# Kernel optimization log

Hardware: AMD Instinct MI355X
Metric: run time of the kernel (lower is better)

The kernel has to match this reference:

```python
import jax, jax.numpy as jnp
import numpy as np

VOCAB = 32000
ROUTE_BIAS = 10.0  # weight on the deterministic one-hot route vs mu logits


def setup_inputs() -> dict:
    key = jax.random.key(0)
    k1, k2, k3, k4, k5, k6 = jax.random.split(key, 6)
    B, S, H = 2, 4096, 1024
    E, Ie = 8, 512  # intermediate_size=4096 -> expert_intermediate=512, fused dim=2*Ie=1024
    return {
        "hidden_states": jax.random.normal(k1, (B, S, H), dtype=jnp.float32),
        "token_ids": jax.random.randint(k2, (B, S), 0, VOCAB),
        "mu": jax.random.normal(k3, (B, S, H), dtype=jnp.float32),
        "gate_up_proj": jax.random.normal(k4, (E, H, 2 * Ie), dtype=jnp.float32) * 0.02,
        "down_proj": jax.random.normal(k5, (E, Ie, H), dtype=jnp.float32) * 0.02,
        "mu_router_w": jax.random.normal(k6, (E, H), dtype=jnp.float32) * 0.02,
    }


def reference(hidden_states, token_ids, mu, gate_up_proj, down_proj, mu_router_w):
    B, S, H = hidden_states.shape
    E, _, F2 = gate_up_proj.shape
    Ie = F2 // 2
    N = B * S

    # deterministic token->expert routing, optionally perturbed by mu logits
    token_to_expert = jnp.arange(VOCAB, dtype=jnp.int32) % E
    base_expert = token_to_expert[jnp.clip(token_ids, 0, VOCAB - 1)]      # [B,S]
    mu_logits = jnp.einsum('bsh,eh->bse', mu, mu_router_w)                 # [B,S,E]
    combined = jax.nn.one_hot(base_expert, E, dtype=mu_logits.dtype) * ROUTE_BIAS + mu_logits
    expert_ids = jnp.argmax(combined, axis=-1).reshape(N)                  # [N]

    x = hidden_states.reshape(N, H)
    tok = jnp.arange(N)

    # compute per-expert GEMM then select per-token expert output
    # (same math as gathering the full weight slab per token, without the
    #  N*H*2Ie gathered-weight blowup of the original torch code)
    gu_all = jnp.einsum('nh,ehf->enf', x, gate_up_proj)                    # [E,N,2Ie]
    gu = gu_all[expert_ids, tok]                                           # [N,2Ie]
    gate, up = gu[:, :Ie], gu[:, Ie:]
    inter = jax.nn.silu(gate) * up                                         # [N,Ie]

    z_all = jnp.einsum('ni,eih->enh', inter, down_proj)                    # [E,N,H]
    out = z_all[expert_ids, tok].reshape(B, S, H)
    return out
```

## Files before the change

kernel.cpp:

```cpp
#include <hip/hip_runtime.h>
#include <hip/hip_bf16.h>
#include <stdint.h>

typedef __bf16 bf16x8 __attribute__((ext_vector_type(8)));
typedef float f32x4 __attribute__((ext_vector_type(4)));

#define ROUTE_BIAS_F 10.0f
#define VOCAB_SZ 32000

__device__ __forceinline__ unsigned short f2bf(float f) {
    union { float f; unsigned u; } v; v.f = f;
    unsigned u = v.u;
    unsigned r = u + 0x7FFFu + ((u >> 16) & 1u);
    return (unsigned short)(r >> 16);
}
__device__ __forceinline__ float bf2f(unsigned short s) {
    union { unsigned u; float f; } v; v.u = ((unsigned)s) << 16;
    return v.f;
}
__device__ __forceinline__ void ld16(const unsigned short* g, unsigned short* l) {
    __builtin_amdgcn_global_load_lds(
        (const __attribute__((address_space(1))) void*)g,
        (__attribute__((address_space(3))) void*)l, 16, 0, 0);
}

__global__ void k_prep(const float* __restrict__ hidden, const float* __restrict__ mu,
                       const int* __restrict__ tok_ids, const float* __restrict__ rw,
                       unsigned short* __restrict__ xb, int* __restrict__ eids,
                       int H, int N) {
    int lane = threadIdx.x & 63;
    int wv   = threadIdx.x >> 6;
    int tok  = blockIdx.x * 4 + wv;
    if (tok >= N) return;
    const float4* hp = (const float4*)(hidden + (size_t)tok * H);
    const float4* mp = (const float4*)(mu + (size_t)tok * H);
    const float4* rp = (const float4*)rw;
    ushort4* xp = (ushort4*)(xb + (size_t)tok * H);
    int H4 = H >> 2;
    float acc[8];
#pragma unroll
    for (int e = 0; e < 8; ++e) acc[e] = 0.f;
#pragma unroll
    for (int j = 0; j < 4; ++j) {
        int idx = lane + 64 * j;
        float4 h4 = hp[idx];
        ushort4 o;
        o.x = f2bf(h4.x); o.y = f2bf(h4.y); o.z = f2bf(h4.z); o.w = f2bf(h4.w);
        xp[idx] = o;
        float4 m4 = mp[idx];
#pragma unroll
        for (int e = 0; e < 8; ++e) {
            float4 w4 = rp[e * H4 + idx];
            acc[e] += m4.x * w4.x + m4.y * w4.y + m4.z * w4.z + m4.w * w4.w;
        }
    }
#pragma unroll
    for (int e = 0; e < 8; ++e) {
        float v = acc[e];
#pragma unroll
        for (int off = 32; off > 0; off >>= 1) v += __shfl_xor(v, off);
        acc[e] = v;
    }
    if (lane == 0) {
        int t = tok_ids[tok];
        if (t < 0) t = 0;
        if (t > VOCAB_SZ - 1) t = VOCAB_SZ - 1;
        int be = t % 8;
        float best = -1e30f; int bi = 0;
#pragma unroll
        for (int e = 0; e < 8; ++e) {
            float v = acc[e] + (e == be ? ROUTE_BIAS_F : 0.f);
            if (v > best) { best = v; bi = e; }
        }
        eids[tok] = bi;
    }
}

__global__ __launch_bounds__(256) void k_transpose_all(
        const float* __restrict__ gup, const float* __restrict__ dnp,
        unsigned short* __restrict__ wgut, unsigned short* __restrict__ wdnt,
        int H, int F2, int Ie) {
    __shared__ float tile[64][65];
    int z = blockIdx.z;
    const float* inp; unsigned short* outp; int R, C;
    if (z < 8) { R = H; C = F2; inp = gup + (size_t)z * R * C;       outp = wgut + (size_t)z * R * C; }
    else       { R = Ie; C = H; inp = dnp + (size_t)(z - 8) * R * C; outp = wdnt + (size_t)(z - 8) * R * C; }
    int c0 = blockIdx.x * 64, r0 = blockIdx.y * 64;
    if (r0 >= R) return;
    int tid = threadIdx.x;
    int tr = tid >> 4;
    int tc = (tid & 15) * 4;
#pragma unroll
    for (int p = 0; p < 4; ++p) {
        float4 v = *(const float4*)&inp[(size_t)(r0 + tr + 16 * p) * C + c0 + tc];
        tile[tr + 16 * p][tc + 0] = v.x;
        tile[tr + 16 * p][tc + 1] = v.y;
        tile[tr + 16 * p][tc + 2] = v.z;
        tile[tr + 16 * p][tc + 3] = v.w;
    }
    __syncthreads();
#pragma unroll
    for (int p = 0; p < 4; ++p) {
        int c = tr + 16 * p;
        ushort4 o;
        o.x = f2bf(tile[tc + 0][c]);
        o.y = f2bf(tile[tc + 1][c]);
        o.z = f2bf(tile[tc + 2][c]);
        o.w = f2bf(tile[tc + 3][c]);
        *(ushort4*)&outp[(size_t)(c0 + c) * R + r0 + tc] = o;
    }
}

__global__ void k_count(const int* __restrict__ eids,
                        int* __restrict__ blockcnt, int N) {
    __shared__ int cnt[8];
    int tid = threadIdx.x;
    if (tid < 8) cnt[tid] = 0;
    __syncthreads();
    int tok = blockIdx.x * 256 + tid;
    int lane = tid & 63;
    int eid = (tok < N) ? eids[tok] : -1;
#pragma unroll
    for (int e = 0; e < 8; ++e) {
        unsigned long long m = __ballot(eid == e);
        if (lane == 0 && m) atomicAdd(&cnt[e], __popcll(m));
    }
    __syncthreads();
    if (tid < 8) blockcnt[blockIdx.x * 8 + tid] = cnt[tid];
}

__global__ void k_scan(const int* __restrict__ blockcnt,
                       int* __restrict__ counts, int* __restrict__ base_,
                       int* __restrict__ offs, int NB) {
    __shared__ int tot[8];
    int lane = threadIdx.x;
    int e = lane >> 3, g = lane & 7;
    int v[4];
    int s = 0;
#pragma unroll
    for (int i = 0; i < 4; ++i) { v[i] = s; s += blockcnt[(g * 4 + i) * 8 + e]; }
    int inc = s;
#pragma unroll
    for (int d = 1; d < 8; d <<= 1) {
        int t = __shfl_up(inc, d);
        if (g >= d) inc += t;
    }
    int excl = inc - s;
#pragma unroll
    for (int i = 0; i < 4; ++i) offs[(g * 4 + i) * 8 + e] = excl + v[i];
    if (g == 7) { counts[e] = inc; tot[e] = inc; }
    __syncthreads();
    if (lane == 0) {
        int s2 = 0;
#pragma unroll
        for (int i = 0; i < 8; ++i) { base_[i] = s2; s2 += tot[i]; }
    }
}

__global__ void k_scatter(const int* __restrict__ eids,
                          const int* __restrict__ offs,
                          int* __restrict__ list, int N) {
    __shared__ int wavecnt[4][8];
    int tid = threadIdx.x;
    int lane = tid & 63, wv = tid >> 6;
    int tok = blockIdx.x * 256 + tid;
    int eid = (tok < N) ? eids[tok] : -1;
    unsigned long long below = (1ull << lane) - 1ull;
    int myrank = 0;
#pragma unroll
    for (int e = 0; e < 8; ++e) {
        unsigned long long m = __ballot(eid == e);
        if (lane == 0) wavecnt[wv][e] = __popcll(m);
        if (eid == e) myrank = __popcll(m & below);
    }
    __syncthreads();
    if (eid >= 0) {
        int pre = 0;
        for (int w = 0; w < wv; ++w) pre += wavecnt[w][eid];
        int pos = offs[blockIdx.x * 8 + eid] + pre + myrank;
        list[eid * N + pos] = tok;
    }
}

#define TM 128
#define TN 128
#define TK 64

__global__ __launch_bounds__(256, 2) void k_gemm_gateup(
    const unsigned short* __restrict__ X,
    const unsigned short* __restrict__ Wt,
    unsigned short* __restrict__ IT,
    const int* __restrict__ counts, const int* __restrict__ base_,
    const int* __restrict__ list, int N, int H, int Ie) {
    int bid = blockIdx.x;
    int e = bid & 7;
    int t = bid >> 3;
    int nt = t & 7;
    int slot = t >> 3;
    int cnt = counts[e];
    int F2 = 2 * Ie;
    int b = base_[e];
    int nt64 = nt * 64;

    __shared__ __align__(16) unsigned short As[2][TM * TK];
    __shared__ __align__(16) unsigned short Bs[2][TN * TK];

    int tid = threadIdx.x;
    int lane = tid & 63, wv = tid >> 6;
    int wr = (wv >> 1) * 64;
    int wc = (wv & 1) * 64;

    int rowg = lane >> 3;
    int sl   = (lane & 7) ^ rowg;

    const unsigned short* bg[4];
#pragma unroll
    for (int i = 0; i < 4; ++i) {
        int r = wv * 32 + i * 8 + rowg;
        int wrow = (r & 1) * Ie + nt64 + (r >> 1);
        bg[i] = Wt + ((size_t)e * F2 + wrow) * H + sl * 8;
    }

    int q = lane >> 4, m = lane & 15;
    int sw = m & 7;
    int nk = H / TK;

    for (int mt = slot; mt * TM < cnt; mt += 8) {
        int m0 = mt * TM;

        const unsigned short* ag[4];
#pragma unroll
        for (int i = 0; i < 4; ++i) {
            int r = wv * 32 + i * 8 + rowg;
            int gr = m0 + r;
            int tokrow = (gr < cnt) ? list[e * N + gr] : 0;
            ag[i] = X + (size_t)tokrow * H + sl * 8;
        }

        f32x4 acc[4][4];
#pragma unroll
        for (int i = 0; i < 4; ++i)
#pragma unroll
            for (int j = 0; j < 4; ++j) acc[i][j] = (f32x4)(0.f);

#pragma unroll
        for (int i = 0; i < 4; ++i) ld16(ag[i], &As[0][(wv * 32 + i * 8) * TK]);
#pragma unroll
        for (int i = 0; i < 4; ++i) ld16(bg[i], &Bs[0][(wv * 32 + i * 8) * TK]);
        __syncthreads();

        int cur = 0;
        for (int t_ = 0; t_ < nk; ++t_) {
            if (t_ + 1 < nk) {
                int k1 = (t_ + 1) * TK;
#pragma unroll
                for (int i = 0; i < 4; ++i) ld16(ag[i] + k1, &As[cur ^ 1][(wv * 32 + i * 8) * TK]);
#pragma unroll
                for (int i = 0; i < 4; ++i) ld16(bg[i] + k1, &Bs[cur ^ 1][(wv * 32 + i * 8) * TK]);
            }
            const unsigned short* Ac = As[cur];
            const unsigned short* Bc = Bs[cur];
            __builtin_amdgcn_s_setprio(1);
#pragma unroll
            for (int ks = 0; ks < TK; ks += 32) {
                int kc = ks >> 3;
                int ck = ((kc + q) ^ sw) << 3;
                bf16x8 af[4], bfr[4];
#pragma unroll
                for (int im = 0; im < 4; ++im)
                    af[im] = *(const bf16x8*)&Ac[(wr + m + im * 16) * TK + ck];
#pragma unroll
                for (int in_ = 0; in_ < 4; ++in_)
                    bfr[in_] = *(const bf16x8*)&Bc[(wc + m + in_ * 16) * TK + ck];
#pragma unroll
                for (int im = 0; im < 4; ++im)
#pragma unroll
                    for (int in_ = 0; in_ < 4; ++in_)
                        acc[im][in_] = __builtin_amdgcn_mfma_f32_16x16x32_bf16(
                            af[im], bfr[in_], acc[im][in_], 0, 0, 0);
            }
            __builtin_amdgcn_s_setprio(0);
            __syncthreads();
            cur ^= 1;
        }

#pragma unroll
        for (int im = 0; im < 4; ++im) {
#pragma unroll
            for (int j = 0; j < 4; ++j) {
                int row = wr + im * 16 + q * 4 + j;
                int gr = m0 + row;
#pragma unroll
                for (int in_ = 0; in_ < 4; ++in_) {
                    float v = acc[im][in_][j];
                    float u = __shfl_xor(v, 1);
                    float g = v;
                    float s = g / (1.f + __expf(-g));
                    float res = s * u;
                    if (!(lane & 1) && gr < cnt) {
                        int oc = nt64 + ((wc + in_ * 16 + m) >> 1);
                        IT[(size_t)(b + gr) * Ie + oc] = f2bf(res);
                    }
                }
            }
        }
    }
}

__global__ __launch_bounds__(256, 3) void k_gemm_down(
    const unsigned short* __restrict__ IT,
    const unsigned short* __restrict__ Wt,
    float* __restrict__ OUT,
    const int* __restrict__ counts, const int* __restrict__ base_,
    const int* __restrict__ list, int N, int Ie, int H) {
    int bid = blockIdx.x;
    int e = bid & 7;
    int t = bid >> 3;
    int nt = t & 7;
    int slot = t >> 3;
    int cnt = counts[e];
    int n0 = nt * TN;
    int b = base_[e];

    __shared__ __align__(16) unsigned short As[TM * TK];
    __shared__ __align__(16) unsigned short Bs[TN * TK];

    int tid = threadIdx.x;
    int lane = tid & 63, wv = tid >> 6;
    int wr = (wv >> 1) * 64;
    int wc = (wv & 1) * 64;

    int rowg = lane >> 3;
    int sl   = (lane & 7) ^ rowg;

    const unsigned short* We = Wt + ((size_t)e * H + n0) * Ie;
    const unsigned short* bg[4];
#pragma unroll
    for (int i = 0; i < 4; ++i) {
        int r = wv * 32 + i * 8 + rowg;
        bg[i] = We + (size_t)r * Ie + sl * 8;
    }

    int q = lane >> 4, m = lane & 15;
    int sw = m & 7;

    for (int mt = slot; mt * TM < cnt; mt += 8) {
        int m0 = mt * TM;

        const unsigned short* ag[4];
#pragma unroll
        for (int i = 0; i < 4; ++i) {
            int r = wv * 32 + i * 8 + rowg;
            int gr = m0 + r;
            int arow = (gr < cnt) ? (b + gr) : b;
            ag[i] = IT + (size_t)arow * Ie + sl * 8;
        }

        f32x4 acc[4][4];
#pragma unroll
        for (int i = 0; i < 4; ++i)
#pragma unroll
            for (int j = 0; j < 4; ++j) acc[i][j] = (f32x4)(0.f);

        for (int k0 = 0; k0 < Ie; k0 += TK) {
#pragma unroll
            for (int i = 0; i < 4; ++i)
                ld16(ag[i] + k0, &As[(wv * 32 + i * 8) * TK]);
#pragma unroll
            for (int i = 0; i < 4; ++i)
                ld16(bg[i] + k0, &Bs[(wv * 32 + i * 8) * TK]);
            __syncthreads();
#pragma unroll
            for (int ks = 0; ks < TK; ks += 32) {
                int kc = ks >> 3;
                int ck = ((kc + q) ^ sw) << 3;
                bf16x8 af[4], bfr[4];
#pragma unroll
                for (int im = 0; im < 4; ++im)
                    af[im] = *(const bf16x8*)&As[(wr + m + im * 16) * TK + ck];
#pragma unroll
                for (int in_ = 0; in_ < 4; ++in_)
                    bfr[in_] = *(const bf16x8*)&Bs[(wc + m + in_ * 16) * TK + ck];
#pragma unroll
                for (int im = 0; im < 4; ++im)
#pragma unroll
                    for (int in_ = 0; in_ < 4; ++in_)
                        acc[im][in_] = __builtin_amdgcn_mfma_f32_16x16x32_bf16(
                            af[im], bfr[in_], acc[im][in_], 0, 0, 0);
            }
            __syncthreads();
        }

#pragma unroll
        for (int im = 0; im < 4; ++im) {
#pragma unroll
            for (int j = 0; j < 4; ++j) {
                int row = wr + im * 16 + q * 4 + j;
                int gr = m0 + row;
                if (gr < cnt) {
                    int tok = list[e * N + gr];
                    float* orow = OUT + (size_t)tok * H + n0;
#pragma unroll
                    for (int in_ = 0; in_ < 4; ++in_) {
                        int col = wc + in_ * 16 + m;
                        orow[col] = acc[im][in_][j];
                    }
                }
            }
        }
    }
}

extern "C" void kernel_launch(void* const* d_in, const int* in_sizes, int n_in,
                              void* d_out, int out_size, void* d_ws, size_t ws_size,
                              hipStream_t stream) {
    const float* hidden   = (const float*)d_in[0];
    const int*   tok_ids  = (const int*)d_in[1];
    const float* mu       = (const float*)d_in[2];
    const float* gup      = (const float*)d_in[3];
    const float* dnp      = (const float*)d_in[4];
    const float* rw       = (const float*)d_in[5];
    float* out = (float*)d_out;

    int N  = in_sizes[1];
    int H  = in_sizes[0] / N;
    int E  = in_sizes[5] / H;
    int F2 = in_sizes[3] / (E * H);
    int Ie = F2 / 2;

    int NB = (N + 255) / 256;

    char* ws = (char*)d_ws;
    size_t o = 0;
    auto alloc = [&](size_t sz) {
        size_t r = o;
        o += (sz + 255) & ~(size_t)255;
        return r;
    };
    int* counts   = (int*)(ws + alloc((size_t)E * 4));
    int* base_    = (int*)(ws + alloc((size_t)E * 4));
    int* eids     = (int*)(ws + alloc((size_t)N * 4));
    int* blockcnt = (int*)(ws + alloc((size_t)NB * 8 * 4));
    int* offs     = (int*)(ws + alloc((size_t)NB * 8 * 4));
    int* list     = (int*)(ws + alloc((size_t)E * N * 4));
    unsigned short* xb   = (unsigned short*)(ws + alloc((size_t)N * H * 2));
    unsigned short* wgut = (unsigned short*)(ws + alloc((size_t)E * F2 * H * 2));
    unsigned short* wdnt = (unsigned short*)(ws + alloc((size_t)E * H * Ie * 2));
    unsigned short* it   = (unsigned short*)(ws + alloc((size_t)N * Ie * 2));

    k_prep<<<dim3((N + 3) / 4), dim3(256), 0, stream>>>(hidden, mu, tok_ids, rw, xb, eids, H, N);

    k_transpose_all<<<dim3(16, 16, 16), dim3(256), 0, stream>>>(gup, dnp, wgut, wdnt, H, F2, Ie);

    k_count<<<dim3(NB), dim3(256), 0, stream>>>(eids, blockcnt, N);
    k_scan<<<dim3(1), dim3(64), 0, stream>>>(blockcnt, counts, base_, offs, NB);
    k_scatter<<<dim3(NB), dim3(256), 0, stream>>>(eids, offs, list, N);

    k_gemm_gateup<<<dim3(E * (Ie / 64) * 8), dim3(256), 0, stream>>>(
        xb, wgut, it, counts, base_, list, N, H, Ie);

    k_gemm_down<<<dim3(E * (H / TN) * 8), dim3(256), 0, stream>>>(
        it, wdnt, out, counts, base_, list, N, Ie, H);
}
```

Before: 239.1 us.

## Prefetch two K-tiles ahead with register-staged fragments in both MoE GEMMs

Both GEMM kernels now issue global-to-LDS loads two tiles ahead. They wait with an explicit vmcnt count instead of a full syncthreads, load all fragments for the tile into registers, then refill the freed LDS buffer before running the MFMAs. The down-projection kernel gains double-buffered LDS and its occupancy hint drops from 3 to 2 blocks per CU. The aim is to hide global load latency behind MFMA work, at the cost of more registers and LDS per block.

```diff
diff --git a/kernel.cpp b/kernel.cpp
--- a/kernel.cpp
+++ b/kernel.cpp
@@ -13,10 +13,6 @@
     unsigned u = v.u;
     unsigned r = u + 0x7FFFu + ((u >> 16) & 1u);
     return (unsigned short)(r >> 16);
-}
-__device__ __forceinline__ float bf2f(unsigned short s) {
-    union { unsigned u; float f; } v; v.u = ((unsigned)s) << 16;
-    return v.f;
 }
 __device__ __forceinline__ void ld16(const unsigned short* g, unsigned short* l) {
     __builtin_amdgcn_global_load_lds(
@@ -244,45 +240,54 @@
             for (int j = 0; j < 4; ++j) acc[i][j] = (f32x4)(0.f);
 
 #pragma unroll
-        for (int i = 0; i < 4; ++i) ld16(ag[i], &As[0][(wv * 32 + i * 8) * TK]);
-#pragma unroll
-        for (int i = 0; i < 4; ++i) ld16(bg[i], &Bs[0][(wv * 32 + i * 8) * TK]);
-        __syncthreads();
-
-        int cur = 0;
+        for (int i = 0; i < 4; ++i) ld16(ag[i],      &As[0][(wv * 32 + i * 8) * TK]);
+#pragma unroll
+        for (int i = 0; i < 4; ++i) ld16(bg[i],      &Bs[0][(wv * 32 + i * 8) * TK]);
+#pragma unroll
+        for (int i = 0; i < 4; ++i) ld16(ag[i] + TK, &As[1][(wv * 32 + i * 8) * TK]);
+#pragma unroll
+        for (int i = 0; i < 4; ++i) ld16(bg[i] + TK, &Bs[1][(wv * 32 + i * 8) * TK]);
+
         for (int t_ = 0; t_ < nk; ++t_) {
-            if (t_ + 1 < nk) {
-                int k1 = (t_ + 1) * TK;
-#pragma unroll
-                for (int i = 0; i < 4; ++i) ld16(ag[i] + k1, &As[cur ^ 1][(wv * 32 + i * 8) * TK]);
-#pragma unroll
-                for (int i = 0; i < 4; ++i) ld16(bg[i] + k1, &Bs[cur ^ 1][(wv * 32 + i * 8) * TK]);
+            asm volatile("s_waitcnt vmcnt(8)" ::: "memory");
+            __builtin_amdgcn_s_barrier();
+
+            const unsigned short* Ac = As[t_ & 1];
+            const unsigned short* Bc = Bs[t_ & 1];
+            bf16x8 af[2][4], bfr[2][4];
+#pragma unroll
+            for (int s = 0; s < 2; ++s) {
+                int ck = (((s * 4) + q) ^ sw) << 3;
+#pragma unroll
+                for (int im = 0; im < 4; ++im)
+                    af[s][im] = *(const bf16x8*)&Ac[(wr + m + im * 16) * TK + ck];
+#pragma unroll
+                for (int in_ = 0; in_ < 4; ++in_)
+                    bfr[s][in_] = *(const bf16x8*)&Bc[(wc + m + in_ * 16) * TK + ck];
             }
-            const unsigned short* Ac = As[cur];
-            const unsigned short* Bc = Bs[cur];
+            asm volatile("s_waitcnt lgkmcnt(0)" ::: "memory");
+            __builtin_amdgcn_s_barrier();
+
+            int tn = t_ + 2; if (tn > nk - 1) tn = nk - 1;
+            int kk = tn * TK;
+#pragma unroll
+            for (int i = 0; i < 4; ++i) ld16(ag[i] + kk, &As[t_ & 1][(wv * 32 + i * 8) * TK]);
+#pragma unroll
+            for (int i = 0; i < 4; ++i) ld16(bg[i] + kk, &Bs[t_ & 1][(wv * 32 + i * 8) * TK]);
+
             __builtin_amdgcn_s_setprio(1);
 #pragma unroll
-            for (int ks = 0; ks < TK; ks += 32) {
-                int kc = ks >> 3;
-                int ck = ((kc + q) ^ sw) << 3;
-                bf16x8 af[4], bfr[4];
-#pragma unroll
-                for (int im = 0; im < 4; ++im)
-                    af[im] = *(const bf16x8*)&Ac[(wr + m + im * 16) * TK + ck];
-#pragma unroll
-                for (int in_ = 0; in_ < 4; ++in_)
-                    bfr[in_] = *(const bf16x8*)&Bc[(wc + m + in_ * 16) * TK + ck];
+            for (int s = 0; s < 2; ++s)
 #pragma unroll
                 for (int im = 0; im < 4; ++im)
 #pragma unroll
                     for (int in_ = 0; in_ < 4; ++in_)
                         acc[im][in_] = __builtin_amdgcn_mfma_f32_16x16x32_bf16(
-                            af[im], bfr[in_], acc[im][in_], 0, 0, 0);
-            }
+                            af[s][im], bfr[s][in_], acc[im][in_], 0, 0, 0);
             __builtin_amdgcn_s_setprio(0);
-            __syncthreads();
-            cur ^= 1;
-        }
+        }
+        asm volatile("s_waitcnt vmcnt(0)" ::: "memory");
+        __builtin_amdgcn_s_barrier();
 
 #pragma unroll
         for (int im = 0; im < 4; ++im) {
@@ -307,7 +312,7 @@
     }
 }
 
-__global__ __launch_bounds__(256, 3) void k_gemm_down(
+__global__ __launch_bounds__(256, 2) void k_gemm_down(
     const unsigned short* __restrict__ IT,
     const unsigned short* __restrict__ Wt,
     float* __restrict__ OUT,
@@ -322,8 +327,8 @@
     int n0 = nt * TN;
     int b = base_[e];
 
-    __shared__ __align__(16) unsigned short As[TM * TK];
-    __shared__ __align__(16) unsigned short Bs[TN * TK];
+    __shared__ __align__(16) unsigned short As[2][TM * TK];
+    __shared__ __align__(16) unsigned short Bs[2][TN * TK];
 
     int tid = threadIdx.x;
     int lane = tid & 63, wv = tid >> 6;
@@ -343,6 +348,7 @@
 
     int q = lane >> 4, m = lane & 15;
     int sw = m & 7;
+    int nk = Ie / TK;
 
     for (int mt = slot; mt * TM < cnt; mt += 8) {
         int m0 = mt * TM;
@@ -362,34 +368,55 @@
 #pragma unroll
             for (int j = 0; j < 4; ++j) acc[i][j] = (f32x4)(0.f);
 
-        for (int k0 = 0; k0 < Ie; k0 += TK) {
-#pragma unroll
-            for (int i = 0; i < 4; ++i)
-                ld16(ag[i] + k0, &As[(wv * 32 + i * 8) * TK]);
-#pragma unroll
-            for (int i = 0; i < 4; ++i)
-                ld16(bg[i] + k0, &Bs[(wv * 32 + i * 8) * TK]);
-            __syncthreads();
-#pragma unroll
-            for (int ks = 0; ks < TK; ks += 32) {
-                int kc = ks >> 3;
-                int ck = ((kc + q) ^ sw) << 3;
-                bf16x8 af[4], bfr[4];
+#pragma unroll
+        for (int i = 0; i < 4; ++i) ld16(ag[i],      &As[0][(wv * 32 + i * 8) * TK]);
+#pragma unroll
+        for (int i = 0; i < 4; ++i) ld16(bg[i],      &Bs[0][(wv * 32 + i * 8) * TK]);
+#pragma unroll
+        for (int i = 0; i < 4; ++i) ld16(ag[i] + TK, &As[1][(wv * 32 + i * 8) * TK]);
+#pragma unroll
+        for (int i = 0; i < 4; ++i) ld16(bg[i] + TK, &Bs[1][(wv * 32 + i * 8) * TK]);
+
+        for (int t_ = 0; t_ < nk; ++t_) {
+            asm volatile("s_waitcnt vmcnt(8)" ::: "memory");
+            __builtin_amdgcn_s_barrier();
+
+            const unsigned short* Ac = As[t_ & 1];
+            const unsigned short* Bc = Bs[t_ & 1];
+            bf16x8 af[2][4], bfr[2][4];
+#pragma unroll
+            for (int s = 0; s < 2; ++s) {
+                int ck = (((s * 4) + q) ^ sw) << 3;
 #pragma unroll
                 for (int im = 0; im < 4; ++im)
-                    af[im] = *(const bf16x8*)&As[(wr + m + im * 16) * TK + ck];
+                    af[s][im] = *(const bf16x8*)&Ac[(wr + m + im * 16) * TK + ck];
 #pragma unroll
                 for (int in_ = 0; in_ < 4; ++in_)
-                    bfr[in_] = *(const bf16x8*)&Bs[(wc + m + in_ * 16) * TK + ck];
+                    bfr[s][in_] = *(const bf16x8*)&Bc[(wc + m + in_ * 16) * TK + ck];
+            }
+            asm volatile("s_waitcnt lgkmcnt(0)" ::: "memory");
+            __builtin_amdgcn_s_barrier();
+
+            int tn = t_ + 2; if (tn > nk - 1) tn = nk - 1;
+            int kk = tn * TK;
+#pragma unroll
+            for (int i = 0; i < 4; ++i) ld16(ag[i] + kk, &As[t_ & 1][(wv * 32 + i * 8) * TK]);
+#pragma unroll
+            for (int i = 0; i < 4; ++i) ld16(bg[i] + kk, &Bs[t_ & 1][(wv * 32 + i * 8) * TK]);
+
+            __builtin_amdgcn_s_setprio(1);
+#pragma unroll
+            for (int s = 0; s < 2; ++s)
 #pragma unroll
                 for (int im = 0; im < 4; ++im)
 #pragma unroll
                     for (int in_ = 0; in_ < 4; ++in_)
                         acc[im][in_] = __builtin_amdgcn_mfma_f32_16x16x32_bf16(
-                            af[im], bfr[in_], acc[im][in_], 0, 0, 0);
-            }
-            __syncthreads();
-        }
+                            af[s][im], bfr[s][in_], acc[im][in_], 0, 0, 0);
+            __builtin_amdgcn_s_setprio(0);
+        }
+        asm volatile("s_waitcnt vmcnt(0)" ::: "memory");
+        __builtin_amdgcn_s_barrier();
 
 #pragma unroll
         for (int im = 0; im < 4; ++im) {
```

Result: faster. 229.1 us (-4.2%).
